# Performance work log

Measured on AMD Instinct MI355X. Metric: run time of the kernel, lower is better.

The kernel has to match this reference:

```python
import jax, jax.numpy as jnp
import numpy as np

B, L, D, VOCAB, LAYERS = 4, 1024, 512, 32000, 4


def setup_inputs() -> dict:
    key = jax.random.key(0)
    ks = jax.random.split(key, 6)
    s = 0.02
    return {
        "input_ids": jax.random.randint(ks[0], (B, L), 0, VOCAB, dtype=jnp.int32),
        "embed": jax.random.normal(ks[1], (VOCAB, D), dtype=jnp.float32) * s,
        "starter": jax.random.normal(ks[2], (LAYERS, D), dtype=jnp.float32) * s,
        "W": jax.random.normal(ks[3], (LAYERS, 2 * D, 2 * D), dtype=jnp.float32) * s,
        "b": jnp.zeros((LAYERS, 2 * D), dtype=jnp.float32),
        "Wout": jax.random.normal(ks[4], (VOCAB, D), dtype=jnp.float32) * s,
        "bout": jnp.zeros((VOCAB,), dtype=jnp.float32),
    }


def reference(input_ids, embed, starter, W, b, Wout, bout):
    Bsz, Lsz = input_ids.shape
    d = starter.shape[-1]
    x = embed[input_ids]                      # [B, L, D]
    xT = jnp.transpose(x, (1, 0, 2))          # [L, B, D] time-major for scan
    s0 = jnp.broadcast_to(starter[:, None, :], (LAYERS, Bsz, d))  # [layers, B, D]

    def layer_step(x_cur, inp):
        Wi, bi, si = inp                      # Wi [2D,2D] (torch out-in), bi [2D], si [B,D]
        xs = jnp.concatenate([x_cur, si], axis=-1) @ Wi.T + bi    # [B, 2D]
        x_new, s_new = jnp.split(xs, 2, axis=-1)
        return x_new, s_new

    def time_step(s_stack, x_t):
        y, new_s = jax.lax.scan(layer_step, x_t, (W, b, s_stack))
        return new_s, y

    _, ys = jax.lax.scan(time_step, s0, xT)   # ys [L, B, D]
    logits = jnp.einsum('lbd,vd->blv', ys, Wout) + bout           # [B, L, V]
    return logits
```

## Files before the change

kernel.cpp:

```cpp
#include <hip/hip_runtime.h>

typedef unsigned short u16;
typedef unsigned int u32;
typedef __attribute__((ext_vector_type(8))) short bf16x8;
typedef __attribute__((ext_vector_type(4))) float f32x4;
typedef __attribute__((ext_vector_type(8))) u16 u16x8;

__device__ __forceinline__ u16 f2b(float f) {
  u32 u = __builtin_bit_cast(u32, f);
  u += 0x7fffu + ((u >> 16) & 1u);
  return (u16)(u >> 16);
}
__device__ __forceinline__ float b2f(u16 h) {
  u32 u = ((u32)h) << 16;
  return __builtin_bit_cast(float, u);
}
__device__ __forceinline__ f32x4 mfma16(bf16x8 a, bf16x8 b, f32x4 c) {
  return __builtin_amdgcn_mfma_f32_16x16x32_bf16(a, b, c, 0, 0, 0);
}
__device__ __host__ __forceinline__ int pidx(int i, int j) { return i * (i + 1) / 2 + j; }

__global__ __launch_bounds__(256) void cast_w_kernel(const float* __restrict__ W,
                                                     u16* __restrict__ Wb,
                                                     u16* __restrict__ WbT) {
  __shared__ u16 tile[64][65];
  int L = blockIdx.z, R0 = blockIdx.y * 64, C0 = blockIdx.x * 64;
  const float* Wl = W + (size_t)L * (1024 * 1024);
  u16* Wbl = Wb + (size_t)L * (1024 * 1024);
  u16* WbTl = WbT + (size_t)L * (1024 * 1024);
  int tr = threadIdx.x >> 6, tc = threadIdx.x & 63;
  for (int i = 0; i < 16; ++i) {
    int r = tr * 16 + i;
    u16 v = f2b(Wl[(size_t)(R0 + r) * 1024 + C0 + tc]);
    Wbl[(size_t)(R0 + r) * 1024 + C0 + tc] = v;
    tile[r][tc] = v;
  }
  __syncthreads();
  for (int i = 0; i < 16; ++i) {
    int r = tr * 16 + i;
    WbTl[(size_t)(C0 + r) * 1024 + R0 + tc] = tile[tc][r];
  }
}

__global__ __launch_bounds__(256) void cast_f32_bf16_kernel(const float* __restrict__ in,
                                                            u16* __restrict__ out, long n8) {
  long i = (long)blockIdx.x * 256 + threadIdx.x;
  long stride = (long)gridDim.x * 256;
  for (; i < n8; i += stride) {
    const float* s = in + i * 8;
    u16x8 o;
#pragma unroll
    for (int j = 0; j < 8; ++j) o[j] = f2b(s[j]);
    *(u16x8*)(out + i * 8) = o;
  }
}

__global__ __launch_bounds__(256) void gather_e_kernel(const int* __restrict__ ids,
                                                       const float* __restrict__ embed,
                                                       u16* __restrict__ ebf) {
  int row = blockIdx.x * 4 + (threadIdx.x >> 6);
  int lane = threadIdx.x & 63;
  int t = row >> 2, b = row & 3;
  int id = ids[b * 1024 + t];
  const float* src = embed + (size_t)id * 512 + lane * 8;
  u16x8 o;
#pragma unroll
  for (int j = 0; j < 8; ++j) o[j] = f2b(src[j]);
  *(u16x8*)(ebf + (size_t)row * 512 + lane * 8) = o;
}

__global__ __launch_bounds__(256) void init_s0_kernel(const float* __restrict__ starter,
                                                      u16* __restrict__ s0buf) {
  int i = blockIdx.x * 256 + threadIdx.x;
  if (i < 2048) {
    u16 v = f2b(starter[i]);
    for (int b = 0; b < 4; ++b) s0buf[(size_t)b * 2048 + i] = v;
  }
}

__global__ __launch_bounds__(256) void assemble_kernel(const u16* __restrict__ Wb,
                                                       const u16* __restrict__ WbT,
                                                       u16* __restrict__ Pv0, u16* __restrict__ Pt0,
                                                       u16* __restrict__ Rm, u16* __restrict__ Um) {
  int task = blockIdx.y;
  int e = blockIdx.x * 256 + threadIdx.x;
  int r = e >> 9, c = e & 511;
  if (task < 4) {
    int i = task;
    size_t boff = (size_t)pidx(i, i) * 262144 + (size_t)r * 512 + c;
    Pv0[boff] = Wb[(size_t)i * 1048576 + (size_t)(512 + r) * 1024 + 512 + c];
    Pt0[boff] = WbT[(size_t)i * 1048576 + (size_t)(512 + r) * 1024 + 512 + c];
  } else if (task == 4) {
    Rm[(size_t)r * 2048 + 3 * 512 + c] = Wb[(size_t)3 * 1048576 + (size_t)r * 1024 + 512 + c];
  } else {
    Um[(size_t)r * 512 + c] = Wb[(size_t)(512 + r) * 1024 + c];
  }
}

__global__ __launch_bounds__(256) void bias_step_kernel(const float* __restrict__ W,
                                                        const float* __restrict__ bv, int layer,
                                                        const float* __restrict__ hin,
                                                        float* __restrict__ hout,
                                                        float* __restrict__ kvec) {
  int wid = threadIdx.x >> 6, lane = threadIdx.x & 63;
  int gw = blockIdx.x * 4 + wid;
  for (int o = gw; o < 1024; o += 64) {
    const float* row = W + (size_t)layer * 1048576 + (size_t)o * 1024;
    float s = 0.f;
    for (int k = lane; k < 512; k += 64) s += row[k] * hin[k];
    for (int off = 32; off; off >>= 1) s += __shfl_down(s, off);
    if (lane == 0) {
      float v = s + bv[layer * 1024 + o];
      if (o < 512) hout[o] = v;
      else kvec[layer * 512 + (o - 512)] = v;
    }
  }
}

struct G512 { const u16* A; const u16* B; u16* C; u16* CT; int lda, ldb, ldc, ldt; };
struct G512Args { G512 g[8]; };

__global__ __launch_bounds__(256) void gemm512_kernel(G512Args args) {
  G512 d = args.g[blockIdx.z];
  int wid = threadIdx.x >> 6, lane = threadIdx.x & 63;
  int wr = wid >> 1, wc = wid & 1;
  int row0 = blockIdx.y * 64 + wr * 32, col0 = blockIdx.x * 64 + wc * 32;
  int fr = lane & 15, fk = (lane >> 4) * 8;
  f32x4 acc[2][2] = {};
  for (int kk = 0; kk < 512; kk += 32) {
    bf16x8 a[2], b[2];
#pragma unroll
    for (int m = 0; m < 2; ++m)
      a[m] = *(const bf16x8*)(d.A + (size_t)(row0 + m * 16 + fr) * d.lda + kk + fk);
#pragma unroll
    for (int n = 0; n < 2; ++n)
      b[n] = *(const bf16x8*)(d.B + (size_t)(col0 + n * 16 + fr) * d.ldb + kk + fk);
#pragma unroll
    for (int m = 0; m < 2; ++m)
#pragma unroll
      for (int n = 0; n < 2; ++n) acc[m][n] = mfma16(a[m], b[n], acc[m][n]);
  }
  int dr = (lane >> 4) * 4, dc = lane & 15;
  for (int m = 0; m < 2; ++m)
    for (int n = 0; n < 2; ++n)
#pragma unroll
      for (int j = 0; j < 4; ++j) {
        int r = row0 + m * 16 + dr + j, c = col0 + n * 16 + dc;
        u16 v = f2b(acc[m][n][j]);
        d.C[(size_t)r * d.ldc + c] = v;
        if (d.CT) d.CT[(size_t)c * d.ldt + r] = v;
      }
}

__global__ __launch_bounds__(256) void sq_packed_kernel(const u16* __restrict__ Pv,
                                                        const u16* __restrict__ Pt,
                                                        u16* __restrict__ Qv,
                                                        u16* __restrict__ Qt) {
  __shared__ char smem[32768];
  char* As = smem;
  char* Bs = smem + 16384;
  const int ti_[10] = {0, 1, 1, 2, 2, 2, 3, 3, 3, 3};
  const int tj_[10] = {0, 0, 1, 0, 1, 2, 0, 1, 2, 3};
  int t = blockIdx.z;
  int ib = ti_[t], jb = tj_[t];
  int nl = ib - jb + 1;
  int tid = threadIdx.x;
  int wid = tid >> 6, lane = tid & 63;
  int wr = wid >> 1, wc = wid & 1;
  int fr = lane & 15, fkb = (lane >> 4) * 8;
  int rowt = blockIdx.y * 128, colt = blockIdx.x * 128;
  f32x4 acc[4][4] = {};
  for (int lb = 0; lb < nl; ++lb) {
    int l = jb + lb;
    const u16* A = Pv + (size_t)pidx(ib, l) * 262144;
    const u16* B = Pt + (size_t)pidx(l, jb) * 262144;
    for (int kk = 0; kk < 512; kk += 64) {
#pragma unroll
      for (int i = 0; i < 4; ++i) {
        int q = i * 256 + tid;
        int r = q >> 3, kc = (q & 7) * 8;
        int so = (r * 128 + kc * 2) ^ ((r & 7) << 4);
        *(bf16x8*)(As + so) = *(const bf16x8*)(A + (size_t)(rowt + r) * 512 + kk + kc);
        *(bf16x8*)(Bs + so) = *(const bf16x8*)(B + (size_t)(colt + r) * 512 + kk + kc);
      }
      __syncthreads();
#pragma unroll
      for (int kh = 0; kh < 64; kh += 32) {
        bf16x8 a[4], b[4];
#pragma unroll
        for (int m = 0; m < 4; ++m) {
          int row = wr * 64 + m * 16 + fr;
          a[m] = *(const bf16x8*)(As + ((row * 128 + (kh + fkb) * 2) ^ ((row & 7) << 4)));
        }
#pragma unroll
        for (int n = 0; n < 4; ++n) {
          int row = wc * 64 + n * 16 + fr;
          b[n] = *(const bf16x8*)(Bs + ((row * 128 + (kh + fkb) * 2) ^ ((row & 7) << 4)));
        }
#pragma unroll
        for (int m = 0; m < 4; ++m)
#pragma unroll
          for (int n = 0; n < 4; ++n) acc[m][n] = mfma16(a[m], b[n], acc[m][n]);
      }
      __syncthreads();
    }
  }
  size_t obase = (size_t)pidx(ib, jb) * 262144;
  int dr = (lane >> 4) * 4, dc = lane & 15;
  for (int m = 0; m < 4; ++m)
    for (int n = 0; n < 4; ++n)
#pragma unroll
      for (int j = 0; j < 4; ++j) {
        int r = rowt + wr * 64 + m * 16 + dr + j;
        int c = colt + wc * 64 + n * 16 + dc;
        u16 v = f2b(acc[m][n][j]);
        Qv[obase + (size_t)r * 512 + c] = v;
        Qt[obase + (size_t)c * 512 + r] = v;
      }
}

__global__ __launch_bounds__(256) void combine_kernel(u16* __restrict__ xdst,
                                                      const u16* __restrict__ xsrc,
                                                      size_t nstride, const u16* __restrict__ Pk,
                                                      int N) {
  extern __shared__ char smem[];
  int tid = threadIdx.x, wid = tid >> 6, lane = tid & 63;
  int ct = blockIdx.x;
  int g0 = blockIdx.y * 4;
  int i_blk = ct >> 1;
  int Keff = (i_blk + 1) << 9;
  int rowb = Keff << 1;
  int cpr = Keff >> 3;
  for (int rr = 0; rr < 4; ++rr) {
    int row = wid * 4 + rr;
    int n = g0 + (row >> 2);
    if (n > N - 1) n = N - 1;
    const u16* srow = xsrc + (size_t)n * nstride + (size_t)(row & 3) * 2048;
    int rb = row * rowb, sw = (row & 7) << 4;
    for (int c0 = lane; c0 < cpr; c0 += 64) {
      uint4 v = *(const uint4*)(srow + c0 * 8);
      *(uint4*)(smem + ((rb + c0 * 16) ^ sw)) = v;
    }
  }
  __syncthreads();
  int fr = lane & 15, fk8 = (lane >> 4) * 8;
  int colw = ct * 256 + wid * 64;
  size_t cl[4];
#pragma unroll
  for (int n = 0; n < 4; ++n) cl[n] = (size_t)((colw + n * 16 + fr) & 511) * 512;
  f32x4 acc[4] = {};
  int asw = (fr & 7) << 4;
  for (int jb = 0; jb <= i_blk; ++jb) {
    const u16* Pb = Pk + (size_t)(i_blk * (i_blk + 1) / 2 + jb) * 262144;
    int kg0 = jb << 9;
#pragma unroll 4
    for (int kk = 0; kk < 512; kk += 32) {
      int kf = kk + fk8;
      int aoff = fr * rowb + (kg0 + kf) * 2;
      bf16x8 a = *(const bf16x8*)(smem + (aoff ^ asw));
#pragma unroll
      for (int n = 0; n < 4; ++n) {
        bf16x8 b = *(const bf16x8*)(Pb + cl[n] + kf);
        acc[n] = mfma16(a, b, acc[n]);
      }
    }
  }
  int dr = (lane >> 4) * 4, dc = lane & 15;
#pragma unroll
  for (int n = 0; n < 4; ++n) {
    int col = colw + n * 16 + dc;
#pragma unroll
    for (int j = 0; j < 4; ++j) {
      int fro = dr + j;
      int nd = g0 + (fro >> 2);
      if (nd > N - 1) nd = N - 1;
      u16* drow = xdst + (size_t)nd * nstride + (size_t)(fro & 3) * 2048 + col;
      *drow = f2b(acc[n][j] + b2f(*drow));
    }
  }
}

template <bool OUT_BF16, bool PERM, bool ADD_PREV, bool HAS_BIAS, bool SWZ>
__global__ __launch_bounds__(256) void gemm128_kernel(
    const u16* __restrict__ A, int lda, const u16* __restrict__ B, int ldb, int K,
    void* __restrict__ C, int ldc,
    const float* __restrict__ bias, const float* __restrict__ prev, int ldp) {
  __shared__ char smem[32768];
  char* As = smem;
  char* Bs = smem + 16384;
  int tid = threadIdx.x;
  int wid = tid >> 6, lane = tid & 63;
  int wr = wid >> 1, wc = wid & 1;
  int fr = lane & 15, fkb = (lane >> 4) * 8;
  int rowt, colt;
  if (SWZ) {
    int bid = blockIdx.x;
    int lin = (bid & 7) * 1000 + (bid >> 3);
    rowt = (lin & 31) * 128;
    colt = (lin >> 5) * 128;
  } else {
    rowt = blockIdx.y * 128;
    colt = blockIdx.x * 128;
  }
  f32x4 acc[4][4] = {};
  for (int kk = 0; kk < K; kk += 64) {
#pragma unroll
    for (int i = 0; i < 4; ++i) {
      int q = i * 256 + tid;
      int r = q >> 3, kc = (q & 7) * 8;
      int so = (r * 128 + kc * 2) ^ ((r & 7) << 4);
      *(bf16x8*)(As + so) = *(const bf16x8*)(A + (size_t)(rowt + r) * lda + kk + kc);
      *(bf16x8*)(Bs + so) = *(const bf16x8*)(B + (size_t)(colt + r) * ldb + kk + kc);
    }
    __syncthreads();
#pragma unroll
    for (int kh = 0; kh < 64; kh += 32) {
      bf16x8 a[4], b[4];
#pragma unroll
      for (int m = 0; m < 4; ++m) {
        int row = wr * 64 + m * 16 + fr;
        a[m] = *(const bf16x8*)(As + ((row * 128 + (kh + fkb) * 2) ^ ((row & 7) << 4)));
      }
#pragma unroll
      for (int n = 0; n < 4; ++n) {
        int row = wc * 64 + n * 16 + fr;
        b[n] = *(const bf16x8*)(Bs + ((row * 128 + (kh + fkb) * 2) ^ ((row & 7) << 4)));
      }
#pragma unroll
      for (int m = 0; m < 4; ++m)
#pragma unroll
        for (int n = 0; n < 4; ++n) acc[m][n] = mfma16(a[m], b[n], acc[m][n]);
    }
    __syncthreads();
  }
  int dr = (lane >> 4) * 4, dc = lane & 15;
  if (PERM && !OUT_BF16) {
    float* sred = (float*)smem;
    for (int ph = 0; ph < 2; ++ph) {
      __syncthreads();
#pragma unroll
      for (int mm = 0; mm < 2; ++mm) {
        int m = ph * 2 + mm;
        int lr = wr * 32 + mm * 16 + dr;
#pragma unroll
        for (int n = 0; n < 4; ++n) {
          int lc = wc * 64 + n * 16 + dc;
#pragma unroll
          for (int j = 0; j < 4; ++j) sred[(lr + j) * 128 + lc] = acc[m][n][j];
        }
      }
      __syncthreads();
#pragma unroll
      for (int it = 0; it < 8; ++it) {
        int lr = it * 8 + (tid >> 5);
        int chunk = tid & 31;
        f32x4 v = *(f32x4*)&sred[lr * 128 + chunk * 4];
        int r = rowt + (lr < 32 ? ph * 32 + lr : 64 + ph * 32 + (lr - 32));
        int orow = (r & 3) * 1024 + (r >> 2);
        int c = colt + chunk * 4;
        if (HAS_BIAS) {
          v[0] += bias[c]; v[1] += bias[c + 1]; v[2] += bias[c + 2]; v[3] += bias[c + 3];
        }
        *(f32x4*)((float*)C + (size_t)orow * ldc + c) = v;
      }
    }
  } else {
    for (int m = 0; m < 4; ++m)
      for (int n = 0; n < 4; ++n) {
        int c = colt + wc * 64 + n * 16 + dc;
        float bvv = HAS_BIAS ? bias[c] : 0.f;
#pragma unroll
        for (int j = 0; j < 4; ++j) {
          int r = rowt + wr * 64 + m * 16 + dr + j;
          float v = acc[m][n][j] + bvv;
          if (ADD_PREV) v += prev[(size_t)r * ldp + c];
          int orow = PERM ? ((r & 3) * 1024 + (r >> 2)) : r;
          if (OUT_BF16) ((u16*)C)[(size_t)orow * ldc + c] = f2b(v);
          else ((float*)C)[(size_t)orow * ldc + c] = v;
        }
      }
  }
}

static inline size_t alignup(size_t x) { return (x + 255) & ~(size_t)255; }

extern "C" void kernel_launch(void* const* d_in, const int* in_sizes, int n_in,
                              void* d_out, int out_size, void* d_ws, size_t ws_size,
                              hipStream_t stream) {
  const int* ids = (const int*)d_in[0];
  const float* embed = (const float*)d_in[1];
  const float* starter = (const float*)d_in[2];
  const float* W = (const float*)d_in[3];
  const float* bvec = (const float*)d_in[4];
  const float* Wout = (const float*)d_in[5];
  const float* bout = (const float*)d_in[6];
  float* out = (float*)d_out;

  const size_t SLOT = 2621440;
  char* p = (char*)d_ws;
  auto alloc = [&](size_t bytes) { char* q = p; p += alignup(bytes); return q; };
  u16* Pv = (u16*)alloc(9 * SLOT * 2);
  u16* Pt = (u16*)alloc(9 * SLOT * 2);
  u16* Wbf = (u16*)alloc(8388608);
  u16* WbT = (u16*)alloc(8388608);
  u16* X2 = (u16*)alloc(524288);  u16* X2T = (u16*)alloc(524288);
  u16* X3 = (u16*)alloc(524288);  u16* X3T = (u16*)alloc(524288);
  u16* P1 = (u16*)alloc(524288);  u16* P1T = (u16*)alloc(524288);
  u16* P2 = (u16*)alloc(524288);  u16* P2T = (u16*)alloc(524288);
  u16* P3 = (u16*)alloc(524288);  u16* P3T = (u16*)alloc(524288);
  u16* Um = (u16*)alloc(2097152);
  u16* Rm = (u16*)alloc(2097152);
  u16* Qm = (u16*)alloc(524288);
  u16* ebf = (u16*)alloc(4194304);
  u16* s0buf = (u16*)alloc(16384 + 16777216);
  u16* xbuf = s0buf + 8192;
  float* kvec = (float*)alloc(8192);
  float* h0 = (float*)alloc(2048);
  float* h1 = (float*)alloc(2048);
  if ((size_t)(p - (char*)d_ws) > ws_size) return;
  u16* WoutB = Pt;
  float* yacc = (float*)Wbf;
  u16* ybf = WbT;

  hipMemsetAsync(h0, 0, 2048, stream);

  cast_w_kernel<<<dim3(16, 16, 4), 256, 0, stream>>>(W, Wbf, WbT);
  gather_e_kernel<<<1024, 256, 0, stream>>>(ids, embed, ebf);
  init_s0_kernel<<<8, 256, 0, stream>>>(starter, s0buf);
  assemble_kernel<<<dim3(1024, 6), 256, 0, stream>>>(Wbf, WbT, Pv, Pt, Rm, Um);

  {
    const float* hin = h0;
    float* hout = h1;
    for (int l = 0; l < 4; ++l) {
      bias_step_kernel<<<16, 256, 0, stream>>>(W, bvec, l, hin, hout, kvec);
      float* t = (float*)hin; hin = hout; hout = t;
    }
  }
  const float* cvec = h0;

  auto wb = [&](int i) { return Wbf + (size_t)i * 1048576; };
  auto wbt = [&](int i) { return WbT + (size_t)i * 1048576; };
  const size_t Apos = 0, Cpos = (size_t)512 * 1024;
  auto pvblk = [&](int i, int j) { return Pv + (size_t)pidx(i, j) * 262144; };
  auto ptblk = [&](int i, int j) { return Pt + (size_t)pidx(i, j) * 262144; };

  {
    G512Args a{};
    int n = 0;
    auto add = [&](const u16* A_, int lda, const u16* B_, int ldb, u16* C_, int ldc, u16* CT_, int ldt) {
      a.g[n++] = G512{A_, B_, C_, CT_, lda, ldb, ldc, ldt};
    };
    add(wb(1) + Apos, 1024, wbt(0) + Apos, 1024, X2, 512, X2T, 512);
    add(wb(1) + Apos, 1024, wbt(0) + Cpos, 1024, P1, 512, P1T, 512);
    add(wb(2) + Apos, 1024, wbt(1) + Cpos, 1024, P3, 512, P3T, 512);
    add(wb(1) + Cpos, 1024, wbt(0) + Cpos, 1024, pvblk(1, 0), 512, ptblk(1, 0), 512);
    add(wb(2) + Cpos, 1024, wbt(1) + Cpos, 1024, pvblk(2, 1), 512, ptblk(2, 1), 512);
    add(wb(3) + Apos, 1024, wbt(2) + Cpos, 1024, Rm + 2 * 512, 2048, nullptr, 0);
    add(wb(3) + Cpos, 1024, wbt(2) + Cpos, 1024, pvblk(3, 2), 512, ptblk(3, 2), 512);
    add(wb(1) + Cpos, 1024, wbt(0) + Apos, 1024, Um + (size_t)1 * 262144, 512, nullptr, 0);
    gemm512_kernel<<<dim3(8, 8, 8), 256, 0, stream>>>(a);
  }
  {
    G512Args a{};
    int n = 0;
    auto add = [&](const u16* A_, int lda, const u16* B_, int ldb, u16* C_, int ldc, u16* CT_, int ldt) {
      a.g[n++] = G512{A_, B_, C_, CT_, lda, ldb, ldc, ldt};
    };
    add(wb(2) + Apos, 1024, X2T, 512, X3, 512, X3T, 512);
    add(wb(2) + Apos, 1024, P1T, 512, P2, 512, P2T, 512);
    add(wb(2) + Cpos, 1024, P1T, 512, pvblk(2, 0), 512, ptblk(2, 0), 512);
    add(wb(3) + Apos, 1024, P3T, 512, Rm + 512, 2048, nullptr, 0);
    add(wb(3) + Cpos, 1024, P3T, 512, pvblk(3, 1), 512, ptblk(3, 1), 512);
    add(wb(2) + Cpos, 1024, X2T, 512, Um + (size_t)2 * 262144, 512, nullptr, 0);
    gemm512_kernel<<<dim3(8, 8, 6), 256, 0, stream>>>(a);
  }
  {
    G512Args a{};
    int n = 0;
    auto add = [&](const u16* A_, int lda, const u16* B_, int ldb, u16* C_, int ldc, u16* CT_, int ldt) {
      a.g[n++] = G512{A_, B_, C_, CT_, lda, ldb, ldc, ldt};
    };
    add(wb(3) + Apos, 1024, X3T, 512, Qm, 512, nullptr, 0);
    add(wb(3) + Apos, 1024, P2T, 512, Rm, 2048, nullptr, 0);
    add(wb(3) + Cpos, 1024, P2T, 512, pvblk(3, 0), 512, ptblk(3, 0), 512);
    add(wb(3) + Cpos, 1024, X3T, 512, Um + (size_t)3 * 262144, 512, nullptr, 0);
    gemm512_kernel<<<dim3(8, 8, 4), 256, 0, stream>>>(a);
  }

  for (int s = 0; s < 8; ++s)
    sq_packed_kernel<<<dim3(4, 4, 10), 256, 0, stream>>>(
        Pv + (size_t)s * SLOT, Pt + (size_t)s * SLOT,
        Pv + (size_t)(s + 1) * SLOT, Pt + (size_t)(s + 1) * SLOT);

  cast_f32_bf16_kernel<<<4096, 256, 0, stream>>>(Wout, WoutB, 32000L * 512 / 8);

  gemm128_kernel<true, false, false, true, false><<<dim3(16, 32), 256, 0, stream>>>(
      ebf, 512, Um, 512, 512, (void*)xbuf, 2048, kvec, nullptr, 0);

  {
    hipFuncSetAttribute((const void*)combine_kernel,
                        hipFuncAttributeMaxDynamicSharedMemorySize, 65536);
    combine_kernel<<<dim3(8, 1), 256, 65536, stream>>>(xbuf, s0buf, (size_t)8192, Pv, 1);
    for (int k = 0; k <= 8; ++k) {
      int h = 1 << k, step = 2 << k;
      int p0 = step - 1;
      int N = 1024 >> (k + 1);
      combine_kernel<<<dim3(8, (N + 3) / 4), 256, 65536, stream>>>(
          xbuf + (size_t)p0 * 8192, xbuf + (size_t)(p0 - h) * 8192,
          (size_t)step * 8192, Pv + (size_t)k * SLOT, N);
    }
    for (int d = 9; d >= 1; --d) {
      int h = 1 << (d - 1), step = 1 << d;
      int p0 = 3 * h - 1;
      int N = (1024 >> d) - 1;
      combine_kernel<<<dim3(8, (N + 3) / 4), 256, 65536, stream>>>(
          xbuf + (size_t)p0 * 8192, xbuf + (size_t)(p0 - h) * 8192,
          (size_t)step * 8192, Pv + (size_t)(d - 1) * SLOT, N);
    }
  }

  gemm128_kernel<false, false, false, false, false><<<dim3(4, 32), 256, 0, stream>>>(
      s0buf, 2048, Rm, 2048, 2048, (void*)yacc, 512, nullptr, nullptr, 0);
  gemm128_kernel<true, false, true, true, false><<<dim3(4, 32), 256, 0, stream>>>(
      ebf, 512, Qm, 512, 512, (void*)ybf, 512, cvec, yacc, 512);

  gemm128_kernel<false, true, false, true, true><<<dim3(8000), 256, 0, stream>>>(
      ybf, 512, WoutB, 512, 512, (void*)out, 32000, bout, nullptr, 0);
}
```

Before: 1.823 ms.

## Retile scan-tree combine as 128x128 MFMA GEMM with K-streamed LDS staging

The combine kernel used to stage a 16-row slab of the source state in 64KB of dynamic LDS and have each wave do a 16x64 output strip. It is replaced by a 128x128 tile GEMM that streams K in 64-wide chunks through 16KB of static LDS and computes 4x4 MFMA fragments per wave. The aim is more reuse of the P-matrix operand loads and higher MFMA density, and the smaller LDS footprint should allow more resident blocks. Small-N tree levels now waste most of each 128-row tile, and rows past the end are masked on store. The logits GEMM's final f32 stores also become nontemporal to reduce cache pollution.

```diff
diff --git a/kernel.cpp b/kernel.cpp
--- a/kernel.cpp
+++ b/kernel.cpp
@@ -219,65 +219,67 @@
       }
 }
 
-__global__ __launch_bounds__(256) void combine_kernel(u16* __restrict__ xdst,
-                                                      const u16* __restrict__ xsrc,
-                                                      size_t nstride, const u16* __restrict__ Pk,
-                                                      int N) {
-  extern __shared__ char smem[];
-  int tid = threadIdx.x, wid = tid >> 6, lane = tid & 63;
-  int ct = blockIdx.x;
-  int g0 = blockIdx.y * 4;
-  int i_blk = ct >> 1;
+__global__ __launch_bounds__(256) void gemm_tree_kernel(u16* __restrict__ xdst,
+                                                        const u16* __restrict__ xsrc,
+                                                        size_t nstride,
+                                                        const u16* __restrict__ Pv, int N) {
+  __shared__ char As[16384];
+  int tid = threadIdx.x;
+  int wid = tid >> 6, lane = tid & 63;
+  int wr = wid >> 1, wc = wid & 1;
+  int fr = lane & 15, fkb = (lane >> 4) * 8;
+  int rowt = blockIdx.y * 128, colt = blockIdx.x * 128;
+  int i_blk = colt >> 9;
   int Keff = (i_blk + 1) << 9;
-  int rowb = Keff << 1;
-  int cpr = Keff >> 3;
-  for (int rr = 0; rr < 4; ++rr) {
-    int row = wid * 4 + rr;
-    int n = g0 + (row >> 2);
-    if (n > N - 1) n = N - 1;
-    const u16* srow = xsrc + (size_t)n * nstride + (size_t)(row & 3) * 2048;
-    int rb = row * rowb, sw = (row & 7) << 4;
-    for (int c0 = lane; c0 < cpr; c0 += 64) {
-      uint4 v = *(const uint4*)(srow + c0 * 8);
-      *(uint4*)(smem + ((rb + c0 * 16) ^ sw)) = v;
-    }
-  }
-  __syncthreads();
-  int fr = lane & 15, fk8 = (lane >> 4) * 8;
-  int colw = ct * 256 + wid * 64;
-  size_t cl[4];
-#pragma unroll
-  for (int n = 0; n < 4; ++n) cl[n] = (size_t)((colw + n * 16 + fr) & 511) * 512;
-  f32x4 acc[4] = {};
-  int asw = (fr & 7) << 4;
-  for (int jb = 0; jb <= i_blk; ++jb) {
-    const u16* Pb = Pk + (size_t)(i_blk * (i_blk + 1) / 2 + jb) * 262144;
-    int kg0 = jb << 9;
-#pragma unroll 4
-    for (int kk = 0; kk < 512; kk += 32) {
-      int kf = kk + fk8;
-      int aoff = fr * rowb + (kg0 + kf) * 2;
-      bf16x8 a = *(const bf16x8*)(smem + (aoff ^ asw));
-#pragma unroll
-      for (int n = 0; n < 4; ++n) {
-        bf16x8 b = *(const bf16x8*)(Pb + cl[n] + kf);
-        acc[n] = mfma16(a, b, acc[n]);
-      }
-    }
+  size_t bl[4];
+#pragma unroll
+  for (int n = 0; n < 4; ++n) bl[n] = (size_t)((colt + wc * 64 + n * 16 + fr) & 511) * 512;
+  f32x4 acc[4][4] = {};
+  for (int kk = 0; kk < Keff; kk += 64) {
+#pragma unroll
+    for (int i = 0; i < 4; ++i) {
+      int q = i * 256 + tid;
+      int r = q >> 3, kc = (q & 7) * 8;
+      int gr = rowt + r;
+      int nn = gr >> 2;
+      if (nn > N - 1) nn = N - 1;
+      int so = (r * 128 + kc * 2) ^ ((r & 7) << 4);
+      *(bf16x8*)(As + so) =
+          *(const bf16x8*)(xsrc + (size_t)nn * nstride + (size_t)(gr & 3) * 2048 + kk + kc);
+    }
+    __syncthreads();
+    const u16* Pb = Pv + (size_t)pidx(i_blk, kk >> 9) * 262144 + (kk & 511);
+#pragma unroll
+    for (int kh = 0; kh < 64; kh += 32) {
+      bf16x8 a[4], b[4];
+#pragma unroll
+      for (int m = 0; m < 4; ++m) {
+        int row = wr * 64 + m * 16 + fr;
+        a[m] = *(const bf16x8*)(As + ((row * 128 + (kh + fkb) * 2) ^ ((row & 7) << 4)));
+      }
+#pragma unroll
+      for (int n = 0; n < 4; ++n) b[n] = *(const bf16x8*)(Pb + bl[n] + kh + fkb);
+#pragma unroll
+      for (int m = 0; m < 4; ++m)
+#pragma unroll
+        for (int n = 0; n < 4; ++n) acc[m][n] = mfma16(a[m], b[n], acc[m][n]);
+    }
+    __syncthreads();
   }
   int dr = (lane >> 4) * 4, dc = lane & 15;
-#pragma unroll
-  for (int n = 0; n < 4; ++n) {
-    int col = colw + n * 16 + dc;
-#pragma unroll
-    for (int j = 0; j < 4; ++j) {
-      int fro = dr + j;
-      int nd = g0 + (fro >> 2);
-      if (nd > N - 1) nd = N - 1;
-      u16* drow = xdst + (size_t)nd * nstride + (size_t)(fro & 3) * 2048 + col;
-      *drow = f2b(acc[n][j] + b2f(*drow));
-    }
-  }
+  int rmax = 4 * N;
+  for (int m = 0; m < 4; ++m)
+    for (int n = 0; n < 4; ++n) {
+      int col = colt + wc * 64 + n * 16 + dc;
+#pragma unroll
+      for (int j = 0; j < 4; ++j) {
+        int gr = rowt + wr * 64 + m * 16 + dr + j;
+        if (gr < rmax) {
+          u16* drow = xdst + (size_t)(gr >> 2) * nstride + (size_t)(gr & 3) * 2048 + col;
+          *drow = f2b(acc[m][n][j] + b2f(*drow));
+        }
+      }
+    }
 }
 
 template <bool OUT_BF16, bool PERM, bool ADD_PREV, bool HAS_BIAS, bool SWZ>
@@ -361,7 +363,7 @@
         if (HAS_BIAS) {
           v[0] += bias[c]; v[1] += bias[c + 1]; v[2] += bias[c + 2]; v[3] += bias[c + 3];
         }
-        *(f32x4*)((float*)C + (size_t)orow * ldc + c) = v;
+        __builtin_nontemporal_store(v, (f32x4*)((float*)C + (size_t)orow * ldc + c));
       }
     }
   } else {
@@ -499,14 +501,12 @@
       ebf, 512, Um, 512, 512, (void*)xbuf, 2048, kvec, nullptr, 0);
 
   {
-    hipFuncSetAttribute((const void*)combine_kernel,
-                        hipFuncAttributeMaxDynamicSharedMemorySize, 65536);
-    combine_kernel<<<dim3(8, 1), 256, 65536, stream>>>(xbuf, s0buf, (size_t)8192, Pv, 1);
+    gemm_tree_kernel<<<dim3(16, 1), 256, 0, stream>>>(xbuf, s0buf, (size_t)8192, Pv, 1);
     for (int k = 0; k <= 8; ++k) {
       int h = 1 << k, step = 2 << k;
       int p0 = step - 1;
       int N = 1024 >> (k + 1);
-      combine_kernel<<<dim3(8, (N + 3) / 4), 256, 65536, stream>>>(
+      gemm_tree_kernel<<<dim3(16, (4 * N + 127) / 128), 256, 0, stream>>>(
           xbuf + (size_t)p0 * 8192, xbuf + (size_t)(p0 - h) * 8192,
           (size_t)step * 8192, Pv + (size_t)k * SLOT, N);
     }
@@ -514,7 +514,7 @@
       int h = 1 << (d - 1), step = 1 << d;
       int p0 = 3 * h - 1;
       int N = (1024 >> d) - 1;
-      combine_kernel<<<dim3(8, (N + 3) / 4), 256, 65536, stream>>>(
+      gemm_tree_kernel<<<dim3(16, (4 * N + 127) / 128), 256, 0, stream>>>(
           xbuf + (size_t)p0 * 8192, xbuf + (size_t)(p0 - h) * 8192,
           (size_t)step * 8192, Pv + (size_t)(d - 1) * SLOT, N);
     }
```

Result: slower. 2.034 ms (+11.6%).
